# Kernel tuning notes

Measured on AMD Instinct MI355X. Metric: run time of the kernel, lower is better.

The kernel has to match this reference:

```python
import jax, jax.numpy as jnp
import numpy as np

WINDOW_SIZE = 11
SIGMA = 1.5
NUM_CHANNEL = 1
C1 = 0.01 ** 2
C2 = 0.03 ** 2


def _gaussian_window(window_size: int, sigma: float, num_channel: int) -> jnp.ndarray:
    x = np.arange(window_size, dtype=np.float32)
    g = np.exp(-((x - window_size // 2) ** 2) / (2.0 * sigma ** 2))
    g = g / g.sum()
    w2d = np.outer(g, g).astype(np.float32)  # [K, K]
    # OIHW depthwise kernel: [C, 1, K, K]
    return jnp.asarray(np.broadcast_to(w2d, (num_channel, 1, window_size, window_size)).copy())


def _dwconv(x: jnp.ndarray, window: jnp.ndarray) -> jnp.ndarray:
    k = window.shape[-1]
    pad = k // 2
    return jax.lax.conv_general_dilated(
        x, window,
        window_strides=(1, 1),
        padding=[(pad, pad), (pad, pad)],
        dimension_numbers=("NCHW", "OIHW", "NCHW"),
        feature_group_count=x.shape[1],
    )


def setup_inputs() -> dict:
    key = jax.random.key(0)
    k1, k2 = jax.random.split(key)
    shape = (32, 1, 512, 512)
    X_gt = jax.random.uniform(k1, shape, dtype=jnp.float32)
    X_pred = jax.random.uniform(k2, shape, dtype=jnp.float32)
    return {"X_gt": X_gt, "X_pred": X_pred}


def reference(X_gt, X_pred):
    window = _gaussian_window(WINDOW_SIZE, SIGMA, X_gt.shape[1]).astype(X_gt.dtype)
    mu1 = _dwconv(X_gt, window)
    mu2 = _dwconv(X_pred, window)
    sq_mu1 = mu1 * mu1
    sq_mu2 = mu2 * mu2
    sigma1 = _dwconv(X_gt * X_gt, window) - sq_mu1
    sigma2 = _dwconv(X_pred * X_pred, window) - sq_mu2
    sigma = _dwconv(X_gt * X_pred, window) - mu1 * mu2
    ssim_map = ((2.0 * (mu1 * mu2) + C1) * (2.0 * sigma + C2)) / (
        (sq_mu1 + sq_mu2 + C1) * (sq_mu1 + sq_mu2 + C2)
    )
    # size_average=True -> scalar mean
    return ssim_map.mean()
```

## Files before the change

kernel.cpp:

```cpp
#include <hip/hip_runtime.h>
#include <math.h>

#define IMG_H 512
#define IMG_W 512
#define KW 11
#define RAD 5
#define TW 64
#define TH 32
#define VW 20
#define VSTR 21

#define C1F (0.01f * 0.01f)
#define C2F (0.03f * 0.03f)

__global__ __launch_bounds__(256, 5)
void ssim_fused_kernel(const float* __restrict__ A, const float* __restrict__ B,
                       float* __restrict__ out, float inv_total) {
    __shared__ float4 vA4[TH][VSTR];
    __shared__ float4 vB4[TH][VSTR];
    __shared__ float4 vP4[TH][VSTR];
    __shared__ float wpart[4];

    const int tid = threadIdx.x;
    const int bx = blockIdx.x;
    const int by = blockIdx.y;
    const int img = blockIdx.z;

    float w[KW];
    {
        float s = 0.f;
#pragma unroll
        for (int i = 0; i < KW; ++i) {
            float d = (float)(i - RAD);
            w[i] = expf(-(d * d) / 4.5f);
            s += w[i];
        }
        float inv = 1.0f / s;
#pragma unroll
        for (int i = 0; i < KW; ++i) w[i] *= inv;
    }

    const float* __restrict__ Ai = A + (size_t)img * IMG_H * IMG_W;
    const float* __restrict__ Bi = B + (size_t)img * IMG_H * IMG_W;
    const int basex = bx * TW - 8;
    const int ybase = by * TH - RAD;

    for (int idx = tid; idx < TH * VW; idx += 256) {
        int r = idx / VW;
        int v = idx - r * VW;
        int colf = basex + 4 * v;
        float4 a = make_float4(0.f, 0.f, 0.f, 0.f);
        float4 b = a, p = a;
        if ((unsigned)colf < (unsigned)IMG_W) {
            int gy0 = ybase + r;
            const float* pa = Ai + (size_t)gy0 * IMG_W + colf;
            const float* pb = Bi + (size_t)gy0 * IMG_W + colf;
#pragma unroll
            for (int k = 0; k < KW; ++k) {
                int gy = gy0 + k;
                if ((unsigned)gy < (unsigned)IMG_H) {
                    float4 av = *(const float4*)(pa + (size_t)k * IMG_W);
                    float4 bv = *(const float4*)(pb + (size_t)k * IMG_W);
                    float wk = w[k];
                    a.x += wk * av.x; a.y += wk * av.y; a.z += wk * av.z; a.w += wk * av.w;
                    b.x += wk * bv.x; b.y += wk * bv.y; b.z += wk * bv.z; b.w += wk * bv.w;
                    p.x += wk * (av.x * bv.x); p.y += wk * (av.y * bv.y);
                    p.z += wk * (av.z * bv.z); p.w += wk * (av.w * bv.w);
                }
            }
        }
        vA4[r][v] = a;
        vB4[r][v] = b;
        vP4[r][v] = p;
    }
    __syncthreads();

    float acc = 0.f;
    for (int idx = tid; idx < TH * (TW / 4); idx += 256) {
        int r = idx >> 4;
        int j = idx & 15;
        float fa[20], fb[20], fp[20];
#pragma unroll
        for (int m = 0; m < 5; ++m) {
            float4 t = vA4[r][j + m];
            fa[4 * m] = t.x; fa[4 * m + 1] = t.y; fa[4 * m + 2] = t.z; fa[4 * m + 3] = t.w;
        }
#pragma unroll
        for (int m = 0; m < 5; ++m) {
            float4 t = vB4[r][j + m];
            fb[4 * m] = t.x; fb[4 * m + 1] = t.y; fb[4 * m + 2] = t.z; fb[4 * m + 3] = t.w;
        }
#pragma unroll
        for (int m = 0; m < 5; ++m) {
            float4 t = vP4[r][j + m];
            fp[4 * m] = t.x; fp[4 * m + 1] = t.y; fp[4 * m + 2] = t.z; fp[4 * m + 3] = t.w;
        }
#pragma unroll
        for (int o = 0; o < 4; ++o) {
            float mu1 = 0.f, mu2 = 0.f, sp = 0.f;
#pragma unroll
            for (int k = 0; k < KW; ++k) {
                mu1 += w[k] * fa[3 + o + k];
                mu2 += w[k] * fb[3 + o + k];
                sp  += w[k] * fp[3 + o + k];
            }
            float m12 = mu1 * mu2;
            float sigma = sp - m12;
            float sq = mu1 * mu1 + mu2 * mu2;
            float num = (2.f * m12 + C1F) * (2.f * sigma + C2F);
            float den = (sq + C1F) * (sq + C2F);
            acc += num / den;
        }
    }

#pragma unroll
    for (int off = 32; off > 0; off >>= 1)
        acc += __shfl_down(acc, off, 64);
    int wid = tid >> 6;
    int lane = tid & 63;
    if (lane == 0) wpart[wid] = acc;
    __syncthreads();
    if (tid == 0) {
        float s = (wpart[0] + wpart[1]) + (wpart[2] + wpart[3]);
        atomicAdd(out, s * inv_total);
    }
}

extern "C" void kernel_launch(void* const* d_in, const int* in_sizes, int n_in,
                              void* d_out, int out_size, void* d_ws, size_t ws_size,
                              hipStream_t stream) {
    const float* A = (const float*)d_in[0];
    const float* B = (const float*)d_in[1];
    float* out = (float*)d_out;

    const int total = in_sizes[0];
    const int nimg = total / (IMG_H * IMG_W);

    hipMemsetAsync(d_out, 0, sizeof(float), stream);

    dim3 grid(IMG_W / TW, IMG_H / TH, nimg);
    ssim_fused_kernel<<<grid, 256, 0, stream>>>(A, B, out, 1.0f / (float)total);
}
```

Before: 168.6 us.

## Replace LDS-staged separable conv with register-resident row-sweep per thread

Each thread now owns a 4-wide column group across full image width and sweeps 18 input rows. It computes the horizontal pass from global float4 loads and scatters it into 8 vertical output accumulators held in registers, so shared memory staging and the block barrier go away. Weights are made wave-uniform with readfirstlane so they can sit in scalar registers. The cost is heavy register pressure (96 accumulator floats plus row buffers), occupancy capped at 2 blocks per CU, and redundant neighbor float4 loads that rely on cache, plus 10 extra halo rows per 8 output rows.

Result: faster. 141.0 us (-16.4%).

```diff
diff --git a/kernel.cpp b/kernel.cpp
--- a/kernel.cpp
+++ b/kernel.cpp
@@ -5,26 +5,29 @@
 #define IMG_W 512
 #define KW 11
 #define RAD 5
-#define TW 64
-#define TH 32
-#define VW 20
-#define VSTR 21
+#define T 8
+#define NG (IMG_W / 4)
 
 #define C1F (0.01f * 0.01f)
 #define C2F (0.03f * 0.03f)
 
-__global__ __launch_bounds__(256, 5)
+__device__ __forceinline__ float ssim_px(float mu1, float mu2, float sp) {
+    float m12 = mu1 * mu2;
+    float sigma = sp - m12;
+    float sq = mu1 * mu1 + mu2 * mu2;
+    return ((2.f * m12 + C1F) * (2.f * sigma + C2F)) / ((sq + C1F) * (sq + C2F));
+}
+
+__global__ __launch_bounds__(256, 2)
 void ssim_fused_kernel(const float* __restrict__ A, const float* __restrict__ B,
                        float* __restrict__ out, float inv_total) {
-    __shared__ float4 vA4[TH][VSTR];
-    __shared__ float4 vB4[TH][VSTR];
-    __shared__ float4 vP4[TH][VSTR];
     __shared__ float wpart[4];
 
     const int tid = threadIdx.x;
-    const int bx = blockIdx.x;
-    const int by = blockIdx.y;
-    const int img = blockIdx.z;
+    const int g = tid & (NG - 1);
+    const int rchunk = tid >> 7;
+    const int img = blockIdx.y;
+    const int ybase = blockIdx.x * (2 * T) + rchunk * T;
 
     float w[KW];
     {
@@ -37,80 +40,81 @@
         }
         float inv = 1.0f / s;
 #pragma unroll
-        for (int i = 0; i < KW; ++i) w[i] *= inv;
+        for (int i = 0; i < KW; ++i) {
+            w[i] *= inv;
+            w[i] = __int_as_float(__builtin_amdgcn_readfirstlane(__float_as_int(w[i])));
+        }
     }
 
     const float* __restrict__ Ai = A + (size_t)img * IMG_H * IMG_W;
     const float* __restrict__ Bi = B + (size_t)img * IMG_H * IMG_W;
-    const int basex = bx * TW - 8;
-    const int ybase = by * TH - RAD;
 
-    for (int idx = tid; idx < TH * VW; idx += 256) {
-        int r = idx / VW;
-        int v = idx - r * VW;
-        int colf = basex + 4 * v;
-        float4 a = make_float4(0.f, 0.f, 0.f, 0.f);
-        float4 b = a, p = a;
-        if ((unsigned)colf < (unsigned)IMG_W) {
-            int gy0 = ybase + r;
-            const float* pa = Ai + (size_t)gy0 * IMG_W + colf;
-            const float* pb = Bi + (size_t)gy0 * IMG_W + colf;
+    float4 accA[T], accB[T], accP[T];
+#pragma unroll
+    for (int o = 0; o < T; ++o) {
+        accA[o] = make_float4(0.f, 0.f, 0.f, 0.f);
+        accB[o] = accA[o];
+        accP[o] = accA[o];
+    }
+
+#pragma unroll
+    for (int i = 0; i < T + 2 * RAD; ++i) {
+        int gy = ybase + i - RAD;
+        if (gy >= 0 && gy < IMG_H) {
+            const float* rowA = Ai + (size_t)gy * IMG_W;
+            const float* rowB = Bi + (size_t)gy * IMG_W;
+
+            float fa[20], fb[20];
+#pragma unroll
+            for (int m = 0; m < 5; ++m) {
+                int gm = g + m - 2;
+                float4 va = make_float4(0.f, 0.f, 0.f, 0.f);
+                float4 vb = va;
+                if ((unsigned)gm < (unsigned)NG) {
+                    va = *(const float4*)(rowA + 4 * gm);
+                    vb = *(const float4*)(rowB + 4 * gm);
+                }
+                fa[4 * m] = va.x; fa[4 * m + 1] = va.y; fa[4 * m + 2] = va.z; fa[4 * m + 3] = va.w;
+                fb[4 * m] = vb.x; fb[4 * m + 1] = vb.y; fb[4 * m + 2] = vb.z; fb[4 * m + 3] = vb.w;
+            }
+
+            float4 hA = make_float4(0.f, 0.f, 0.f, 0.f);
+            float4 hB = hA, hP = hA;
 #pragma unroll
             for (int k = 0; k < KW; ++k) {
-                int gy = gy0 + k;
-                if ((unsigned)gy < (unsigned)IMG_H) {
-                    float4 av = *(const float4*)(pa + (size_t)k * IMG_W);
-                    float4 bv = *(const float4*)(pb + (size_t)k * IMG_W);
-                    float wk = w[k];
-                    a.x += wk * av.x; a.y += wk * av.y; a.z += wk * av.z; a.w += wk * av.w;
-                    b.x += wk * bv.x; b.y += wk * bv.y; b.z += wk * bv.z; b.w += wk * bv.w;
-                    p.x += wk * (av.x * bv.x); p.y += wk * (av.y * bv.y);
-                    p.z += wk * (av.z * bv.z); p.w += wk * (av.w * bv.w);
+                float wk = w[k];
+                hA.x += wk * fa[3 + k];  hA.y += wk * fa[4 + k];
+                hA.z += wk * fa[5 + k];  hA.w += wk * fa[6 + k];
+                hB.x += wk * fb[3 + k];  hB.y += wk * fb[4 + k];
+                hB.z += wk * fb[5 + k];  hB.w += wk * fb[6 + k];
+                hP.x += wk * (fa[3 + k] * fb[3 + k]);
+                hP.y += wk * (fa[4 + k] * fb[4 + k]);
+                hP.z += wk * (fa[5 + k] * fb[5 + k]);
+                hP.w += wk * (fa[6 + k] * fb[6 + k]);
+            }
+
+#pragma unroll
+            for (int o = 0; o < T; ++o) {
+                if (i - o >= 0 && i - o < KW) {
+                    float wk = w[i - o];
+                    accA[o].x += wk * hA.x; accA[o].y += wk * hA.y;
+                    accA[o].z += wk * hA.z; accA[o].w += wk * hA.w;
+                    accB[o].x += wk * hB.x; accB[o].y += wk * hB.y;
+                    accB[o].z += wk * hB.z; accB[o].w += wk * hB.w;
+                    accP[o].x += wk * hP.x; accP[o].y += wk * hP.y;
+                    accP[o].z += wk * hP.z; accP[o].w += wk * hP.w;
                 }
             }
         }
-        vA4[r][v] = a;
-        vB4[r][v] = b;
-        vP4[r][v] = p;
     }
-    __syncthreads();
 
     float acc = 0.f;
-    for (int idx = tid; idx < TH * (TW / 4); idx += 256) {
-        int r = idx >> 4;
-        int j = idx & 15;
-        float fa[20], fb[20], fp[20];
 #pragma unroll
-        for (int m = 0; m < 5; ++m) {
-            float4 t = vA4[r][j + m];
-            fa[4 * m] = t.x; fa[4 * m + 1] = t.y; fa[4 * m + 2] = t.z; fa[4 * m + 3] = t.w;
-        }
-#pragma unroll
-        for (int m = 0; m < 5; ++m) {
-            float4 t = vB4[r][j + m];
-            fb[4 * m] = t.x; fb[4 * m + 1] = t.y; fb[4 * m + 2] = t.z; fb[4 * m + 3] = t.w;
-        }
-#pragma unroll
-        for (int m = 0; m < 5; ++m) {
-            float4 t = vP4[r][j + m];
-            fp[4 * m] = t.x; fp[4 * m + 1] = t.y; fp[4 * m + 2] = t.z; fp[4 * m + 3] = t.w;
-        }
-#pragma unroll
-        for (int o = 0; o < 4; ++o) {
-            float mu1 = 0.f, mu2 = 0.f, sp = 0.f;
-#pragma unroll
-            for (int k = 0; k < KW; ++k) {
-                mu1 += w[k] * fa[3 + o + k];
-                mu2 += w[k] * fb[3 + o + k];
-                sp  += w[k] * fp[3 + o + k];
-            }
-            float m12 = mu1 * mu2;
-            float sigma = sp - m12;
-            float sq = mu1 * mu1 + mu2 * mu2;
-            float num = (2.f * m12 + C1F) * (2.f * sigma + C2F);
-            float den = (sq + C1F) * (sq + C2F);
-            acc += num / den;
-        }
+    for (int o = 0; o < T; ++o) {
+        acc += ssim_px(accA[o].x, accB[o].x, accP[o].x);
+        acc += ssim_px(accA[o].y, accB[o].y, accP[o].y);
+        acc += ssim_px(accA[o].z, accB[o].z, accP[o].z);
+        acc += ssim_px(accA[o].w, accB[o].w, accP[o].w);
     }
 
 #pragma unroll
@@ -138,6 +142,6 @@
 
     hipMemsetAsync(d_out, 0, sizeof(float), stream);
 
-    dim3 grid(IMG_W / TW, IMG_H / TH, nimg);
+    dim3 grid(IMG_H / (2 * T), nimg, 1);
     ssim_fused_kernel<<<grid, 256, 0, stream>>>(A, B, out, 1.0f / (float)total);
 }
```

## Stage input rows in shared memory and halve tile height

Applied to the files above, without the earlier changes.

Instead of each thread loading 11 rows of float4 straight from global memory for the vertical pass, the block first stages the tile plus halo into shared memory and runs the vertical convolution from there. The tile height drops from 32 to 16, so each thread handles exactly one output quad and the horizontal loop becomes a single pass. Gaussian weights are made wave-uniform with readfirstlane, and the occupancy hint in launch bounds is removed. This cuts redundant global and L2 traffic, but the halo is now a larger share of each tile, shared memory per block grows, and there are more blocks and atomics.

New measurement: 197.4 us. +17.0%, slower.

```diff
diff --git a/kernel.cpp b/kernel.cpp
--- a/kernel.cpp
+++ b/kernel.cpp
@@ -6,16 +6,19 @@
 #define KW 11
 #define RAD 5
 #define TW 64
-#define TH 32
+#define TH 16
 #define VW 20
+#define SR (TH + 2 * RAD)
 #define VSTR 21
 
 #define C1F (0.01f * 0.01f)
 #define C2F (0.03f * 0.03f)
 
-__global__ __launch_bounds__(256, 5)
+__global__ __launch_bounds__(256)
 void ssim_fused_kernel(const float* __restrict__ A, const float* __restrict__ B,
                        float* __restrict__ out, float inv_total) {
+    __shared__ float4 sA4[SR][VSTR];
+    __shared__ float4 sB4[SR][VSTR];
     __shared__ float4 vA4[TH][VSTR];
     __shared__ float4 vB4[TH][VSTR];
     __shared__ float4 vP4[TH][VSTR];
@@ -37,7 +40,10 @@
         }
         float inv = 1.0f / s;
 #pragma unroll
-        for (int i = 0; i < KW; ++i) w[i] *= inv;
+        for (int i = 0; i < KW; ++i) {
+            w[i] *= inv;
+            w[i] = __int_as_float(__builtin_amdgcn_readfirstlane(__float_as_int(w[i])));
+        }
     }
 
     const float* __restrict__ Ai = A + (size_t)img * IMG_H * IMG_W;
@@ -45,40 +51,48 @@
     const int basex = bx * TW - 8;
     const int ybase = by * TH - RAD;
 
+    for (int idx = tid; idx < SR * VW; idx += 256) {
+        int r = idx / VW;
+        int c = idx - r * VW;
+        int gx = basex + 4 * c;
+        int gy = ybase + r;
+        float4 a = make_float4(0.f, 0.f, 0.f, 0.f);
+        float4 b = a;
+        if ((unsigned)gy < (unsigned)IMG_H && (unsigned)gx < (unsigned)IMG_W) {
+            size_t off = (size_t)gy * IMG_W + gx;
+            a = *(const float4*)(Ai + off);
+            b = *(const float4*)(Bi + off);
+        }
+        sA4[r][c] = a;
+        sB4[r][c] = b;
+    }
+    __syncthreads();
+
     for (int idx = tid; idx < TH * VW; idx += 256) {
-        int r = idx / VW;
-        int v = idx - r * VW;
-        int colf = basex + 4 * v;
+        int r = idx & 15;
+        int c = idx >> 4;
         float4 a = make_float4(0.f, 0.f, 0.f, 0.f);
         float4 b = a, p = a;
-        if ((unsigned)colf < (unsigned)IMG_W) {
-            int gy0 = ybase + r;
-            const float* pa = Ai + (size_t)gy0 * IMG_W + colf;
-            const float* pb = Bi + (size_t)gy0 * IMG_W + colf;
 #pragma unroll
-            for (int k = 0; k < KW; ++k) {
-                int gy = gy0 + k;
-                if ((unsigned)gy < (unsigned)IMG_H) {
-                    float4 av = *(const float4*)(pa + (size_t)k * IMG_W);
-                    float4 bv = *(const float4*)(pb + (size_t)k * IMG_W);
-                    float wk = w[k];
-                    a.x += wk * av.x; a.y += wk * av.y; a.z += wk * av.z; a.w += wk * av.w;
-                    b.x += wk * bv.x; b.y += wk * bv.y; b.z += wk * bv.z; b.w += wk * bv.w;
-                    p.x += wk * (av.x * bv.x); p.y += wk * (av.y * bv.y);
-                    p.z += wk * (av.z * bv.z); p.w += wk * (av.w * bv.w);
-                }
-            }
+        for (int k = 0; k < KW; ++k) {
+            float4 av = sA4[r + k][c];
+            float4 bv = sB4[r + k][c];
+            float wk = w[k];
+            a.x += wk * av.x; a.y += wk * av.y; a.z += wk * av.z; a.w += wk * av.w;
+            b.x += wk * bv.x; b.y += wk * bv.y; b.z += wk * bv.z; b.w += wk * bv.w;
+            p.x += wk * (av.x * bv.x); p.y += wk * (av.y * bv.y);
+            p.z += wk * (av.z * bv.z); p.w += wk * (av.w * bv.w);
         }
-        vA4[r][v] = a;
-        vB4[r][v] = b;
-        vP4[r][v] = p;
+        vA4[r][c] = a;
+        vB4[r][c] = b;
+        vP4[r][c] = p;
     }
     __syncthreads();
 
     float acc = 0.f;
-    for (int idx = tid; idx < TH * (TW / 4); idx += 256) {
-        int r = idx >> 4;
-        int j = idx & 15;
+    {
+        int r = tid >> 4;
+        int j = tid & 15;
         float fa[20], fb[20], fp[20];
 #pragma unroll
         for (int m = 0; m < 5; ++m) {
```
